# Optimization experiments

Hardware: AMD Instinct MI355X
Metric: run time of the kernel (lower is better)

Reference implementation:

```python
import jax, jax.numpy as jnp
import numpy as np

B, E, S = 2, 1024, 2048
H = 16
D_QK = D_V = D_OUT = 1024
NEG = -1e4


def setup_inputs() -> dict:
    key = jax.random.key(0)
    ks = jax.random.split(key, 12)
    q = jax.random.normal(ks[0], (B, E, 1, S), jnp.float32)
    k = jax.random.normal(ks[1], (B, E, 1, S), jnp.float32)
    v = jax.random.normal(ks[2], (B, E, 1, S), jnp.float32)
    # causal qk_mask: (B, src, 1, tgt); src index > tgt index is masked
    causal = jnp.where(jnp.arange(S)[:, None] > jnp.arange(S)[None, :], NEG, 0.0).astype(jnp.float32)
    qk_mask = jnp.broadcast_to(causal[None, :, None, :], (B, S, 1, S))
    k_mask = jnp.zeros((B, S, 1, 1), jnp.float32)
    sc = 1.0 / np.sqrt(E)
    Wq = jax.random.normal(ks[3], (D_QK, E), jnp.float32) * sc
    Wk = jax.random.normal(ks[4], (D_QK, E), jnp.float32) * sc
    Wv = jax.random.normal(ks[5], (D_V, E), jnp.float32) * sc
    Wo = jax.random.normal(ks[6], (D_OUT, D_V), jnp.float32) * sc
    bq = jnp.zeros((D_QK,), jnp.float32)
    bk = jnp.zeros((D_QK,), jnp.float32)
    bv = jnp.zeros((D_V,), jnp.float32)
    bo = jnp.zeros((D_OUT,), jnp.float32)
    return {"q": q, "k": k, "v": v, "qk_mask": qk_mask, "k_mask": k_mask,
            "Wq": Wq, "bq": bq, "Wk": Wk, "bk": bk, "Wv": Wv, "bv": bv,
            "Wo": Wo, "bo": bo}


def reference(q, k, v, qk_mask, k_mask, Wq, bq, Wk, bk, Wv, bv, Wo, bo):
    b, _, _, tq = q.shape
    sk = k.shape[3]
    d_qk, d_v = Wq.shape[0], Wv.shape[0]
    dh, dvh = d_qk // H, d_v // H
    fact = float(dh) ** (-0.5)
    # 1x1 conv projections on (B, C, 1, S) == matmul over channels
    qp = jnp.einsum('oc,bcis->bois', Wq, q) + bq[None, :, None, None]
    kp = jnp.einsum('oc,bcis->bois', Wk, k) + bk[None, :, None, None]
    vp = jnp.einsum('oc,bcis->bois', Wv, v) + bv[None, :, None, None]
    # split heads: channel dim is head-major (contiguous chunks)
    qh = qp[:, :, 0, :].reshape(b, H, dh, tq)
    kh = kp[:, :, 0, :].reshape(b, H, dh, sk)
    vh = vp[:, :, 0, :].reshape(b, H, dvh, sk)
    # scores: (B, H, src, tgt); masks broadcast over heads
    scores = jnp.einsum('bhcq,bhck->bhkq', qh, kh) * fact
    scores = scores + qk_mask[:, None, :, 0, :] + k_mask[:, None, :, 0, 0][..., None]
    w = jax.nn.softmax(scores, axis=2)  # softmax over src (k) axis
    attn = jnp.einsum('bhkq,bhck->bhcq', w, vh).reshape(b, d_v, 1, tq)
    out = jnp.einsum('oc,bcis->bois', Wo, attn) + bo[None, :, None, None]
    return out
```

## Files before the change

### kernel.cpp

```cpp
#include <hip/hip_runtime.h>
#include <hip/hip_bf16.h>
#include <stdint.h>

typedef unsigned short u16;
typedef __attribute__((ext_vector_type(8))) short short8;
typedef __attribute__((ext_vector_type(4))) short short4v;
typedef __attribute__((ext_vector_type(4))) float f32x4;

#define MFMA16(a,b,c) __builtin_amdgcn_mfma_f32_16x16x32_bf16((a),(b),(c),0,0,0)
#define EXP2F(x) __builtin_amdgcn_exp2f(x)

typedef const __attribute__((address_space(1))) void glb_void;
typedef __attribute__((address_space(3))) void lds_void;

__device__ __forceinline__ u16 f2b(float f){
  unsigned u = __float_as_uint(f);
  u += 0x7fffu + ((u>>16)&1u);
  return (u16)(u>>16);
}
__device__ __forceinline__ unsigned pack_bf16(float a, float b){
  __hip_bfloat162 h = __float22bfloat162_rn(make_float2(a,b));
  unsigned u; __builtin_memcpy(&u, &h, 4); return u;
}
__device__ __forceinline__ void gld16(const void* g, void* l){
  __builtin_amdgcn_global_load_lds((glb_void*)g, (lds_void*)l, 16, 0, 0);
}

__device__ __forceinline__ void stage128x64_sw(const u16* g, u16* lds, int gstride, int w, int lane){
  const int sub = lane>>3, c16 = lane&7;
  const int gcol = (c16 ^ sub)<<3;
  #pragma unroll
  for (int i=0;i<4;++i){
    int r0 = (w*4+i)*8;
    gld16(g + (size_t)(r0 + sub)*gstride + gcol, lds + r0*64);
  }
}
__device__ __forceinline__ void stage64x64_sw(const u16* g, u16* lds, int gstride, int w, int lane){
  const int sub = lane>>3, c16 = lane&7;
  const int gcol = (c16 ^ sub)<<3;
  #pragma unroll
  for (int i=0;i<2;++i){
    int r0 = (w*2+i)*8;
    gld16(g + (size_t)(r0 + sub)*gstride + gcol, lds + r0*64);
  }
}
__device__ __forceinline__ const short8* frag64(const u16* lds, int row, int c16){
  return (const short8*)(lds + row*64 + ((c16 ^ (row&7))<<3));
}
__device__ __forceinline__ void stage64x128_sw(const u16* g, u16* lds, int gstride, int w, int lane){
  const int sub = lane>>4, c16 = lane&15;
  #pragma unroll
  for (int i=0;i<4;++i){
    int r0 = (w*4+i)*4;
    int row = r0 + sub;
    gld16(g + (size_t)row*gstride + ((c16 ^ (row&15))<<3), lds + r0*128);
  }
}
__device__ __forceinline__ const short8* frag128(const u16* lds, int row, int c16){
  return (const short8*)(lds + row*128 + ((c16 ^ (row&15))<<3));
}

__global__ __launch_bounds__(256) void prep(
    const float* __restrict__ q, const float* __restrict__ k, const float* __restrict__ v,
    const float* __restrict__ qkm, const float* __restrict__ km,
    const float* __restrict__ Wq, const float* __restrict__ Wk,
    const float* __restrict__ Wv, const float* __restrict__ Wo,
    u16* __restrict__ W16, char* __restrict__ classes,
    u16* __restrict__ qT, u16* __restrict__ kT, u16* __restrict__ vT)
{
  __shared__ __align__(16) float t[64][72];
  const int bx = blockIdx.x, tid = threadIdx.x;
  const int S = 2048, E = 1024, nW = E*E;

  if (bx < 2048){
    const int sel = bx>>9, blk = bx&511;
    const float* src = sel==0?Wq : sel==1?Wk : sel==2?Wv : Wo;
    const float sc = (sel==0) ? 0.18033688f : 1.0f;
    u16* dst = W16 + (size_t)sel*nW;
    int i = (blk*256 + tid)*8;
    float4 a = *(const float4*)(src+i);
    float4 b = *(const float4*)(src+i+4);
    short8 o;
    o[0]=(short)f2b(a.x*sc); o[1]=(short)f2b(a.y*sc); o[2]=(short)f2b(a.z*sc); o[3]=(short)f2b(a.w*sc);
    o[4]=(short)f2b(b.x*sc); o[5]=(short)f2b(b.y*sc); o[6]=(short)f2b(b.z*sc); o[7]=(short)f2b(b.w*sc);
    *(short8*)(dst+i) = o;
  } else if (bx < 4096){
    const int tt = bx - 2048;
    const int b = tt>>10, qi = (tt>>5)&31, ki = tt&31;
    const int k0 = ki*64, q0 = qi*64;
    int az = 1, an = 1;
    #pragma unroll
    for (int p=0;p<4;++p){
      int e = tid + p*256;
      int row = e>>4, c4 = (e&15)*4;
      float kmv = km[(size_t)b*S + k0 + row];
      float4 mv = *(const float4*)&qkm[((size_t)b*S + k0 + row)*S + q0 + c4];
      mv.x += kmv; mv.y += kmv; mv.z += kmv; mv.w += kmv;
      az &= (mv.x==0.f) & (mv.y==0.f) & (mv.z==0.f) & (mv.w==0.f);
      an &= (mv.x<-1e3f) & (mv.y<-1e3f) & (mv.z<-1e3f) & (mv.w<-1e3f);
    }
    const int az_all = __syncthreads_and(az);
    const int an_all = __syncthreads_and(an);
    if (tid==0)
      classes[((size_t)b*32 + qi)*32 + ki] = an_all ? 2 : (az_all ? 0 : 1);
  } else {
    const int tt = bx - 4096;
    const int tensor = tt>>10, r = tt&1023;
    const int b = r>>9, rr = r&511;
    const int c0 = (rr>>5)*64, s0 = (rr&31)*64;
    const float* x = tensor==0 ? q : tensor==1 ? k : v;
    u16* xt = tensor==0 ? qT : tensor==1 ? kT : vT;
    #pragma unroll
    for (int p=0;p<4;++p){
      int e = tid + p*256;
      int row = e>>4, c4 = (e&15)*4;
      *(float4*)&t[row][c4] = *(const float4*)&x[((size_t)b*E + c0 + row)*S + s0 + c4];
    }
    __syncthreads();
    #pragma unroll
    for (int p=0;p<2;++p){
      int e = tid + p*256;
      int row = e>>3, col8 = (e&7)*8;
      short8 o;
      #pragma unroll
      for (int u=0;u<8;++u) o[u] = (short)f2b(t[col8+u][row]);
      *(short8*)&xt[((size_t)b*S + s0 + row)*E + c0 + col8] = o;
    }
  }
}

template<bool F32OUT>
__device__ __forceinline__ void gemm_core(
    const u16* __restrict__ A, const u16* __restrict__ Bt, const float* __restrict__ bias,
    float bscale, void* __restrict__ Cv, size_t cbase, int N, int K, int bias_on_m,
    int m0, int n0, u16* As, u16* Bs)
{
  const int tid = threadIdx.x, w = tid>>6, lane = tid&63;
  const int ln = lane&15, quad = lane>>4;
  const int m0w = (w>>1)*64, n0w = (w&1)*64;
  f32x4 acc[4][4];
  #pragma unroll
  for(int i=0;i<4;++i)
    #pragma unroll
    for(int j=0;j<4;++j) acc[i][j] = f32x4{0.f,0.f,0.f,0.f};

  for (int kc=0; kc<K; kc+=64){
    __syncthreads();
    stage128x64_sw(A  + (size_t)m0*K + kc, As, K, w, lane);
    stage128x64_sw(Bt + (size_t)n0*K + kc, Bs, K, w, lane);
    __syncthreads();
    #pragma unroll
    for (int kk=0; kk<64; kk+=32){
      const int c16 = (kk>>3) + quad;
      short8 af[4], bf[4];
      #pragma unroll
      for (int mt=0;mt<4;++mt) af[mt] = *frag64(As, m0w+mt*16+ln, c16);
      #pragma unroll
      for (int nt=0;nt<4;++nt) bf[nt] = *frag64(Bs, n0w+nt*16+ln, c16);
      #pragma unroll
      for (int mt=0;mt<4;++mt)
        #pragma unroll
        for (int nt=0;nt<4;++nt)
          acc[mt][nt] = MFMA16(af[mt], bf[nt], acc[mt][nt]);
    }
  }
  #pragma unroll
  for (int mt=0;mt<4;++mt){
    #pragma unroll
    for (int nt=0;nt<4;++nt){
      const int col = n0 + n0w + nt*16 + ln;
      const float bn = bias_on_m ? 0.f : bias[col]*bscale;
      #pragma unroll
      for (int r=0;r<4;++r){
        const int row = m0 + m0w + mt*16 + quad*4 + r;
        const float bb = bias_on_m ? bias[row]*bscale : bn;
        const float val = acc[mt][nt][r] + bb;
        const size_t idx = cbase + (size_t)row*N + col;
        if (F32OUT) ((float*)Cv)[idx] = val;
        else        ((u16*)Cv)[idx]   = f2b(val);
      }
    }
  }
}

__global__ __launch_bounds__(256,3) void proj(
    const u16* __restrict__ qT, const u16* __restrict__ kT, const u16* __restrict__ vT,
    const u16* __restrict__ W16,
    const float* __restrict__ bq, const float* __restrict__ bk, const float* __restrict__ bv,
    u16* __restrict__ Qb, u16* __restrict__ Kb, u16* __restrict__ Vb)
{
  __shared__ __align__(16) u16 As[128*64];
  __shared__ __align__(16) u16 Bs[128*64];
  const int bx = blockIdx.x;
  const int zone = bx>>7, r = bx&127;
  const size_t sSE = (size_t)2048*1024;
  const int nW = 1024*1024;
  if (zone < 4){
    const int sel = zone>>1, b = zone&1;
    const int m0 = (r>>3)*128, n0 = (r&7)*128;
    gemm_core<false>((sel? kT : qT) + b*sSE, W16 + (size_t)sel*nW, sel? bk : bq,
                     sel? 1.0f : 0.18033688f, sel? Kb : Qb, b*sSE,
                     1024, 1024, 0, m0, n0, As, Bs);
  } else {
    const int b = zone&1;
    const int m0 = (r>>4)*128, n0 = (r&15)*128;
    gemm_core<false>(W16 + (size_t)2*nW, vT + b*sSE, bv,
                     1.0f, Vb, b*sSE,
                     2048, 1024, 1, m0, n0, As, Bs);
  }
}

__global__ __launch_bounds__(256,4) void gemm_out64(
    const u16* __restrict__ Wo16, const u16* __restrict__ At, const float* __restrict__ bo,
    float* __restrict__ out)
{
  __shared__ __align__(16) u16 As[64*64];
  __shared__ __align__(16) u16 Bs[128*64];
  const int b = blockIdx.z;
  const int m0 = blockIdx.y*64, n0 = blockIdx.x*128;
  const size_t sSE = (size_t)2048*1024;
  const int K = 1024, N = 2048;
  const u16* Bt = At + b*sSE;
  const int tid = threadIdx.x, w = tid>>6, lane = tid&63;
  const int ln = lane&15, quad = lane>>4;
  const int m0w = (w>>1)*32, n0w = (w&1)*64;
  f32x4 acc[2][4];
  #pragma unroll
  for(int i=0;i<2;++i)
    #pragma unroll
    for(int j=0;j<4;++j) acc[i][j] = f32x4{0.f,0.f,0.f,0.f};

  for (int kc=0; kc<K; kc+=64){
    __syncthreads();
    stage64x64_sw (Wo16 + (size_t)m0*K + kc, As, K, w, lane);
    stage128x64_sw(Bt   + (size_t)n0*K + kc, Bs, K, w, lane);
    __syncthreads();
    #pragma unroll
    for (int kk=0; kk<64; kk+=32){
      const int c16 = (kk>>3) + quad;
      short8 af[2], bf[4];
      #pragma unroll
      for (int mt=0;mt<2;++mt) af[mt] = *frag64(As, m0w+mt*16+ln, c16);
      #pragma unroll
      for (int nt=0;nt<4;++nt) bf[nt] = *frag64(Bs, n0w+nt*16+ln, c16);
      #pragma unroll
      for (int mt=0;mt<2;++mt)
        #pragma unroll
        for (int nt=0;nt<4;++nt)
          acc[mt][nt] = MFMA16(af[mt], bf[nt], acc[mt][nt]);
    }
  }
  #pragma unroll
  for (int mt=0;mt<2;++mt){
    #pragma unroll
    for (int nt=0;nt<4;++nt){
      const int col = n0 + n0w + nt*16 + ln;
      #pragma unroll
      for (int r=0;r<4;++r){
        const int row = m0 + m0w + mt*16 + quad*4 + r;
        out[b*sSE + (size_t)row*N + col] = acc[mt][nt][r] + bo[row];
      }
    }
  }
}

__global__ __launch_bounds__(256,2) void attn(
    const u16* __restrict__ Qb, const u16* __restrict__ Kb, const u16* __restrict__ Vb,
    const float* __restrict__ qk_mask, const float* __restrict__ k_mask,
    const char* __restrict__ classes, u16* __restrict__ Ot)
{
  __shared__ __align__(16) u16 Ks[128*64];
  __shared__ __align__(16) u16 Vs[64*128];
  const int x = blockIdx.x;
  const int b = x&1, h = (x>>1)&15;
  const int pp = x>>5, pair = pp>>1, half = pp&1;
  const int tid = threadIdx.x, w = tid>>6, lane = tid&63;
  const int ln = lane&15, quad = lane>>4;
  const int S = 2048;
  const float LOG2E = 1.44269504f, C2 = 16.0f;

  #pragma unroll
  for (int sub=0; sub<2; ++sub){
    const int qt = sub ? pair : (15-pair);
    const int qbase = qt*128 + half*64;
    const int qg = qbase + w*16 + ln;
    short8 qf[2];
    #pragma unroll
    for (int kkI=0;kkI<2;++kkI)
      qf[kkI] = *(const short8*)&Qb[((size_t)b*S + qg)*1024 + h*64 + kkI*32 + quad*8];

    const char* cl = classes + ((size_t)b*32 + qt*2 + half)*32;
    float rs = 0.f;
    f32x4 acc[4];
    #pragma unroll
    for (int ct=0;ct<4;++ct) acc[ct] = f32x4{0.f,0.f,0.f,0.f};

    for (int kt=0; kt<16; ++kt){
      const char c0 = cl[2*kt], c1 = cl[2*kt+1];
      if (c0==2 && c1==2) continue;
      const bool nomask = (c0|c1)==0;
      const int k0 = kt*128;
      __syncthreads();
      stage128x64_sw(Kb + ((size_t)b*S + k0)*1024 + h*64, Ks, 1024, w, lane);
      stage64x128_sw(Vb + ((size_t)b*1024 + h*64)*S + k0, Vs, S, w, lane);
      __syncthreads();

      unsigned pk[8][2];
      #pragma unroll
      for (int t=0;t<8;++t){
        f32x4 s = f32x4{0.f,0.f,0.f,0.f};
        #pragma unroll
        for (int kkI=0;kkI<2;++kkI)
          s = MFMA16(*frag64(Ks, t*16+ln, kkI*4 + quad), qf[kkI], s);
        float e[4];
        if (nomask){
          #pragma unroll
          for (int r=0;r<4;++r) e[r] = EXP2F(s[r] - C2);
        } else {
          #pragma unroll
          for (int r=0;r<4;++r){
            const int kg = k0 + t*16 + quad*4 + r;
            const float m = qk_mask[((size_t)b*S + kg)*S + qg] + k_mask[(size_t)b*S + kg];
            e[r] = EXP2F(fmaf(m, LOG2E, s[r]) - C2);
          }
        }
        rs += (e[0]+e[1]) + (e[2]+e[3]);
        pk[t][0] = pack_bf16(e[0], e[1]);
        pk[t][1] = pack_bf16(e[2], e[3]);
      }
      const int srcA = (quad&1)*32 + ln, srcB = srcA + 16;
      const bool hi = (quad>>1)&1;
      #pragma unroll
      for (int c=0;c<4;++c){
        unsigned a0 = __shfl((int)pk[2*c][0],   srcA, 64);
        unsigned a1 = __shfl((int)pk[2*c][1],   srcA, 64);
        unsigned a2 = __shfl((int)pk[2*c][0],   srcB, 64);
        unsigned a3 = __shfl((int)pk[2*c][1],   srcB, 64);
        unsigned b0 = __shfl((int)pk[2*c+1][0], srcA, 64);
        unsigned b1 = __shfl((int)pk[2*c+1][1], srcA, 64);
        unsigned b2 = __shfl((int)pk[2*c+1][0], srcB, 64);
        unsigned b3 = __shfl((int)pk[2*c+1][1], srcB, 64);
        short8 pf;
        ((unsigned*)&pf)[0] = hi ? b0 : a0;
        ((unsigned*)&pf)[1] = hi ? b1 : a1;
        ((unsigned*)&pf)[2] = hi ? b2 : a2;
        ((unsigned*)&pf)[3] = hi ? b3 : a3;
        #pragma unroll
        for (int ct=0;ct<4;++ct)
          acc[ct] = MFMA16(*frag128(Vs, ct*16+ln, c*4 + quad), pf, acc[ct]);
      }
    }
    rs += __shfl_xor(rs, 16, 64);
    rs += __shfl_xor(rs, 32, 64);
    const float rinv = 1.0f / rs;
    #pragma unroll
    for (int ct=0;ct<4;++ct){
      short4v o4;
      #pragma unroll
      for (int r=0;r<4;++r) o4[r] = (short)f2b(acc[ct][r] * rinv);
      *(short4v*)&Ot[((size_t)b*S + qg)*1024 + h*64 + ct*16 + quad*4] = o4;
    }
  }
}

extern "C" void kernel_launch(void* const* d_in, const int* in_sizes, int n_in,
                              void* d_out, int out_size, void* d_ws, size_t ws_size,
                              hipStream_t stream)
{
  const float* q   = (const float*)d_in[0];
  const float* k   = (const float*)d_in[1];
  const float* v   = (const float*)d_in[2];
  const float* qkm = (const float*)d_in[3];
  const float* km  = (const float*)d_in[4];
  const float* Wq  = (const float*)d_in[5];
  const float* bq  = (const float*)d_in[6];
  const float* Wk  = (const float*)d_in[7];
  const float* bk  = (const float*)d_in[8];
  const float* Wv  = (const float*)d_in[9];
  const float* bv  = (const float*)d_in[10];
  const float* Wo  = (const float*)d_in[11];
  const float* bo  = (const float*)d_in[12];
  float* out = (float*)d_out;

  const size_t nAct = (size_t)2*2048*1024;
  const int   nW   = 1024*1024;

  u16* A0 = (u16*)d_ws;
  u16* A1 = A0 + nAct;
  u16* A2 = A1 + nAct;
  u16* A3 = A2 + nAct;
  u16* A4 = A3 + nAct;
  u16* A5 = A4 + nAct;
  u16* W16 = A5 + nAct;
  char* classes = (char*)(W16 + (size_t)4*nW);
  u16* Wo16 = W16 + (size_t)3*nW;

  dim3 blk(256);
  prep      <<<dim3(7168), blk, 0, stream>>>(q, k, v, qkm, km, Wq, Wk, Wv, Wo,
                                             W16, classes, A0, A1, A2);
  proj      <<<dim3(768),  blk, 0, stream>>>(A0, A1, A2, W16, bq, bk, bv, A3, A4, A5);
  attn      <<<dim3(512),  blk, 0, stream>>>(A3, A4, A5, qkm, km, classes, A0);
  gemm_out64<<<dim3(16,16,2), blk, 0, stream>>>(Wo16, A0, bo, out);
}
```

Baseline: 254.7 us.

## Split attention work across waves by key rows with LDS P exchange and cross-wave reduction

```diff
diff --git a/kernel.cpp b/kernel.cpp
--- a/kernel.cpp
+++ b/kernel.cpp
@@ -271,29 +271,39 @@
 {
   __shared__ __align__(16) u16 Ks[128*64];
   __shared__ __align__(16) u16 Vs[64*128];
+  __shared__ __align__(16) unsigned Ps[4][64*16];
+  __shared__ __align__(16) float xbuf[4][16*68];
+  __shared__ float lbuf[4][64];
   const int x = blockIdx.x;
   const int b = x&1, h = (x>>1)&15;
   const int pp = x>>5, pair = pp>>1, half = pp&1;
   const int tid = threadIdx.x, w = tid>>6, lane = tid&63;
   const int ln = lane&15, quad = lane>>4;
+  const int swz = ((ln>>1)&3)<<2;
   const int S = 2048;
   const float LOG2E = 1.44269504f, C2 = 16.0f;
+  unsigned* Pw = Ps[w];
 
   #pragma unroll
   for (int sub=0; sub<2; ++sub){
     const int qt = sub ? pair : (15-pair);
     const int qbase = qt*128 + half*64;
-    const int qg = qbase + w*16 + ln;
-    short8 qf[2];
-    #pragma unroll
-    for (int kkI=0;kkI<2;++kkI)
-      qf[kkI] = *(const short8*)&Qb[((size_t)b*S + qg)*1024 + h*64 + kkI*32 + quad*8];
+    short8 qf[4][2];
+    #pragma unroll
+    for (int tn=0;tn<4;++tn)
+      #pragma unroll
+      for (int kkI=0;kkI<2;++kkI)
+        qf[tn][kkI] = *(const short8*)&Qb[((size_t)b*S + qbase + tn*16 + ln)*1024 + h*64 + kkI*32 + quad*8];
 
     const char* cl = classes + ((size_t)b*32 + qt*2 + half)*32;
-    float rs = 0.f;
-    f32x4 acc[4];
-    #pragma unroll
-    for (int ct=0;ct<4;++ct) acc[ct] = f32x4{0.f,0.f,0.f,0.f};
+    float rs[4];
+    f32x4 acc[4][4];
+    #pragma unroll
+    for (int ct=0;ct<4;++ct){
+      rs[ct] = 0.f;
+      #pragma unroll
+      for (int tn=0;tn<4;++tn) acc[ct][tn] = f32x4{0.f,0.f,0.f,0.f};
+    }
 
     for (int kt=0; kt<16; ++kt){
       const char c0 = cl[2*kt], c1 = cl[2*kt+1];
@@ -305,60 +315,87 @@
       stage64x128_sw(Vb + ((size_t)b*1024 + h*64)*S + k0, Vs, S, w, lane);
       __syncthreads();
 
-      unsigned pk[8][2];
-      #pragma unroll
-      for (int t=0;t<8;++t){
-        f32x4 s = f32x4{0.f,0.f,0.f,0.f};
+      short8 kf[2][2];
+      #pragma unroll
+      for (int tmI=0;tmI<2;++tmI)
         #pragma unroll
         for (int kkI=0;kkI<2;++kkI)
-          s = MFMA16(*frag64(Ks, t*16+ln, kkI*4 + quad), qf[kkI], s);
-        float e[4];
-        if (nomask){
-          #pragma unroll
-          for (int r=0;r<4;++r) e[r] = EXP2F(s[r] - C2);
-        } else {
-          #pragma unroll
-          for (int r=0;r<4;++r){
-            const int kg = k0 + t*16 + quad*4 + r;
-            const float m = qk_mask[((size_t)b*S + kg)*S + qg] + k_mask[(size_t)b*S + kg];
-            e[r] = EXP2F(fmaf(m, LOG2E, s[r]) - C2);
+          kf[tmI][kkI] = *frag64(Ks, (2*w+tmI)*16+ln, kkI*4+quad);
+
+      #pragma unroll
+      for (int tmI=0;tmI<2;++tmI){
+        const int kgb = k0 + (2*w+tmI)*16 + quad*4;
+        #pragma unroll
+        for (int tn=0;tn<4;++tn){
+          f32x4 s = {0.f,0.f,0.f,0.f};
+          s = MFMA16(kf[tmI][0], qf[tn][0], s);
+          s = MFMA16(kf[tmI][1], qf[tn][1], s);
+          float e[4];
+          if (nomask){
+            #pragma unroll
+            for (int r=0;r<4;++r) e[r] = EXP2F(s[r] - C2);
+          } else {
+            const int qg2 = qbase + tn*16 + ln;
+            #pragma unroll
+            for (int r=0;r<4;++r){
+              const int kg = kgb + r;
+              const float m = qk_mask[((size_t)b*S + kg)*S + qg2] + k_mask[(size_t)b*S + kg];
+              e[r] = EXP2F(fmaf(m, LOG2E, s[r]) - C2);
+            }
           }
+          rs[tn] += (e[0]+e[1]) + (e[2]+e[3]);
+          const int row16 = (tn*16+ln)*16;
+          Pw[row16 + ((tmI*8 + quad*2 + 0) ^ swz)] = pack_bf16(e[0], e[1]);
+          Pw[row16 + ((tmI*8 + quad*2 + 1) ^ swz)] = pack_bf16(e[2], e[3]);
         }
-        rs += (e[0]+e[1]) + (e[2]+e[3]);
-        pk[t][0] = pack_bf16(e[0], e[1]);
-        pk[t][1] = pack_bf16(e[2], e[3]);
       }
-      const int srcA = (quad&1)*32 + ln, srcB = srcA + 16;
-      const bool hi = (quad>>1)&1;
-      #pragma unroll
-      for (int c=0;c<4;++c){
-        unsigned a0 = __shfl((int)pk[2*c][0],   srcA, 64);
-        unsigned a1 = __shfl((int)pk[2*c][1],   srcA, 64);
-        unsigned a2 = __shfl((int)pk[2*c][0],   srcB, 64);
-        unsigned a3 = __shfl((int)pk[2*c][1],   srcB, 64);
-        unsigned b0 = __shfl((int)pk[2*c+1][0], srcA, 64);
-        unsigned b1 = __shfl((int)pk[2*c+1][1], srcA, 64);
-        unsigned b2 = __shfl((int)pk[2*c+1][0], srcB, 64);
-        unsigned b3 = __shfl((int)pk[2*c+1][1], srcB, 64);
-        short8 pf;
-        ((unsigned*)&pf)[0] = hi ? b0 : a0;
-        ((unsigned*)&pf)[1] = hi ? b1 : a1;
-        ((unsigned*)&pf)[2] = hi ? b2 : a2;
-        ((unsigned*)&pf)[3] = hi ? b3 : a3;
-        #pragma unroll
-        for (int ct=0;ct<4;++ct)
-          acc[ct] = MFMA16(*frag128(Vs, ct*16+ln, c*4 + quad), pf, acc[ct]);
+      short8 vf[4], pf[4];
+      #pragma unroll
+      for (int ct=0;ct<4;++ct) vf[ct] = *frag128(Vs, ct*16+ln, w*4 + quad);
+      #pragma unroll
+      for (int tn=0;tn<4;++tn) pf[tn] = *(const short8*)&Pw[(tn*16+ln)*16 + ((quad*4) ^ swz)];
+      #pragma unroll
+      for (int ct=0;ct<4;++ct)
+        #pragma unroll
+        for (int tn=0;tn<4;++tn)
+          acc[ct][tn] = MFMA16(vf[ct], pf[tn], acc[ct][tn]);
+    }
+
+    #pragma unroll
+    for (int tn=0;tn<4;++tn){
+      rs[tn] += __shfl_xor(rs[tn], 16, 64);
+      rs[tn] += __shfl_xor(rs[tn], 32, 64);
+    }
+    if (lane < 16){
+      #pragma unroll
+      for (int tn=0;tn<4;++tn) lbuf[w][tn*16+lane] = rs[tn];
+    }
+    float linv[4];
+    #pragma unroll
+    for (int rr=1; rr<4; ++rr){
+      const int dst = (w+rr)&3;
+      #pragma unroll
+      for (int tn=0;tn<4;++tn)
+        *(float4*)&xbuf[dst][ln*68 + quad*16 + tn*4] = float4{acc[dst][tn][0],acc[dst][tn][1],acc[dst][tn][2],acc[dst][tn][3]};
+      __syncthreads();
+      if (rr==1){
+        #pragma unroll
+        for (int tn=0;tn<4;++tn)
+          linv[tn] = 1.0f / (lbuf[0][tn*16+ln] + lbuf[1][tn*16+ln] + lbuf[2][tn*16+ln] + lbuf[3][tn*16+ln]);
       }
-    }
-    rs += __shfl_xor(rs, 16, 64);
-    rs += __shfl_xor(rs, 32, 64);
-    const float rinv = 1.0f / rs;
-    #pragma unroll
-    for (int ct=0;ct<4;++ct){
+      #pragma unroll
+      for (int tn=0;tn<4;++tn){
+        const float4 vx = *(const float4*)&xbuf[w][ln*68 + quad*16 + tn*4];
+        acc[w][tn][0] += vx.x; acc[w][tn][1] += vx.y; acc[w][tn][2] += vx.z; acc[w][tn][3] += vx.w;
+      }
+      __syncthreads();
+    }
+    #pragma unroll
+    for (int tn=0;tn<4;++tn){
       short4v o4;
       #pragma unroll
-      for (int r=0;r<4;++r) o4[r] = (short)f2b(acc[ct][r] * rinv);
-      *(short4v*)&Ot[((size_t)b*S + qg)*1024 + h*64 + ct*16 + quad*4] = o4;
+      for (int r=0;r<4;++r) o4[r] = (short)f2b(acc[w][tn][r] * linv[tn]);
+      *(short4v*)&Ot[((size_t)b*S + qbase + tn*16 + ln)*1024 + h*64 + w*16 + quad*4] = o4;
     }
   }
 }
```

Result: slower. 393.2 us (+54.4%).
